# Kernel tuning notes

Hardware: AMD Instinct MI355X
Metric: run time of the kernel (lower is better)

The kernel has to match this reference:

```python
import jax, jax.numpy as jnp
import numpy as np

B, K, D = 32768, 64, 64
GAIN = 1.0
LOG_2PI = float(np.log(2.0 * np.pi))


def setup_inputs() -> dict:
    key = jax.random.key(0)
    k1, k2, k3, k4 = jax.random.split(key, 4)
    return {
        "x": jax.random.normal(k1, (B, D), jnp.float32),
        "means_raw": jax.random.normal(k2, (K, D), jnp.float32),
        "scale_raw": jax.random.normal(k3, (K, D, D), jnp.float32),
        "weights_raw": jax.random.normal(k4, (K,), jnp.float32),
    }


def reference(x, means_raw, scale_raw, weights_raw):
    # EqualizedLR reparametrization: w_eff = w * gain / sqrt(fan_in)
    means = means_raw * (GAIN / np.sqrt(K * D))              # [K, D]
    pre = scale_raw * (GAIN / np.sqrt(K * D * D))            # [K, D, D]
    # ExpScaleTril (diag=False): strict lower triangle + exp(diagonal)
    dvec = jnp.exp(jnp.diagonal(pre, axis1=-2, axis2=-1))    # [K, D]
    L = jnp.tril(pre, -1) + dvec[..., :, None] * jnp.eye(D, dtype=pre.dtype)  # [K, D, D]
    # mixture logits -> log weights (EqualizedLR then softmax parametrization)
    logw = jax.nn.log_softmax(weights_raw * (GAIN / np.sqrt(K)), axis=-1)    # [K]

    # Precompute L^{-1} per component (K,D small), then whiten via one big GEMM.
    eye = jnp.broadcast_to(jnp.eye(D, dtype=L.dtype), L.shape)
    Linv = jax.scipy.linalg.solve_triangular(L, eye, lower=True)             # [K, D, D]

    diff = x[:, None, :] - means[None, :, :]                 # [B, K, D]
    z = jnp.einsum('kij,bkj->bki', Linv, diff)               # whitened residuals [B, K, D]
    maha = jnp.sum(z * z, axis=-1)                           # [B, K]
    half_log_det = jnp.sum(jnp.log(dvec), axis=-1)           # [K]
    comp_lp = -0.5 * (maha + D * LOG_2PI) - half_log_det     # [B, K]

    lp = jax.scipy.special.logsumexp(comp_lp + logw, axis=-1)  # [B]
    return -jnp.mean(lp)
```

## Files before the change

kernel.cpp:

```cpp
#include <hip/hip_runtime.h>

#define LOG_2PI 1.8378770664093453f
#define LOG2E   1.4426950408889634f

typedef __attribute__((ext_vector_type(8))) short  short8;
typedef __attribute__((ext_vector_type(4))) float  float4_;
typedef __attribute__((ext_vector_type(4))) unsigned uint4_;

__device__ __forceinline__ unsigned short f2bf(float f) {
  unsigned u = __builtin_bit_cast(unsigned, f);
  u += 0x7fffu + ((u >> 16) & 1u);
  return (unsigned short)(u >> 16);
}
__device__ __forceinline__ float bf2f(unsigned short h) {
  return __builtin_bit_cast(float, ((unsigned)h) << 16);
}
__device__ __forceinline__ unsigned bits(float f) { return __builtin_bit_cast(unsigned, f); }
__device__ __forceinline__ float bitf(unsigned u) { return __builtin_bit_cast(float, u); }
__device__ __forceinline__ unsigned pk2(float lo, float hi) {
  return __builtin_amdgcn_perm(bits(hi), bits(lo), 0x07060302u);
}
__device__ __forceinline__ unsigned pk2r(float lo, float hi) {
  return __builtin_amdgcn_perm(bits(hi) + 0x8000u, bits(lo) + 0x8000u, 0x07060302u);
}
template <int CTRL>
__device__ __forceinline__ float dpp_add(float v) {
  int t = __builtin_amdgcn_mov_dpp(__builtin_bit_cast(int, v), CTRL, 0xf, 0xf, true);
  return v + __builtin_bit_cast(float, t);
}
__device__ __forceinline__ void async16(const void* g, void* l) {
  __builtin_amdgcn_global_load_lds((const __attribute__((address_space(1))) unsigned int*)g,
                                   (__attribute__((address_space(3))) unsigned int*)l, 16, 0, 0);
}


__global__ __launch_bounds__(256) void gmm_setup(
    const float* __restrict__ means_raw, const float* __restrict__ scale_raw,
    const float* __restrict__ weights_raw, unsigned short* __restrict__ Wv,
    float* __restrict__ out)
{
  const int k = blockIdx.x;
  const int t = threadIdx.x;
  const int lane = t & 63;
  const int wv = t >> 6;
  const int q = lane >> 4;
  const int jj = lane & 15;

  if (k == 0 && t == 0) out[0] = 0.0f;

  __shared__ float Plt[64][68];
  __shared__ float Vt[64][68];
  __shared__ __align__(16) unsigned short Vb[64][72];
  __shared__ float Msh[64][65];
  __shared__ float dg[64], rdg[64], mu_s[64], y_s[64], cs_[64];
  __shared__ float beta_s;

  {
    const int i = t >> 2;
    const int c0 = (t & 3) * 16;
    float4_ v4[4];
    const float4_* src = (const float4_*)(scale_raw + (size_t)k * 4096 + i * 64 + c0);
    v4[0] = src[0]; v4[1] = src[1]; v4[2] = src[2]; v4[3] = src[3];
#pragma unroll
    for (int e = 0; e < 16; ++e) {
      const int c = c0 + e;
      const float val = ((const float*)v4)[e] * (1.0f / 512.0f);
      Plt[c][i] = (c < i) ? val : 0.0f;
      if (c == i) { dg[i] = val; rdg[i] = __expf(-val); }
    }
  }
  if (t < 64) mu_s[t] = means_raw[k * 64 + t] * (1.0f / 64.0f);
  __syncthreads();

  {
    const int j = wv * 16 + jj;
    float s[16];
#pragma unroll
    for (int i = 0; i < 16; ++i) s[i] = 0.0f;
#pragma unroll
    for (int m = 0; m < 64; ++m) {
      const float rm = rdg[m];
      float vcand = (m == j) ? rm : -s[m & 15] * rm;
      const float v = __shfl(vcand, (m >> 4) * 16 + jj, 64);
      if (q == (m >> 4)) {
        Vt[j][m] = v;
        Vb[j][m] = f2bf(v);
      }
      const float4_* prow = (const float4_*)&Plt[m][16 * q];
      const float4_ p0 = prow[0], p1 = prow[1], p2 = prow[2], p3 = prow[3];
      s[0]  += p0[0] * v; s[1]  += p0[1] * v; s[2]  += p0[2] * v; s[3]  += p0[3] * v;
      s[4]  += p1[0] * v; s[5]  += p1[1] * v; s[6]  += p1[2] * v; s[7]  += p1[3] * v;
      s[8]  += p2[0] * v; s[9]  += p2[1] * v; s[10] += p2[2] * v; s[11] += p2[3] * v;
      s[12] += p3[0] * v; s[13] += p3[1] * v; s[14] += p3[2] * v; s[15] += p3[3] * v;
    }
  }
  __syncthreads();

  {
    const short8 a0 = *(const short8*)&Vb[16 * wv + jj][8 * q];
    const short8 a1 = *(const short8*)&Vb[16 * wv + jj][8 * q + 32];
#pragma unroll
    for (int t4 = 0; t4 < 4; ++t4) {
      const short8 b0 = *(const short8*)&Vb[jj + 16 * t4][8 * q];
      const short8 b1 = *(const short8*)&Vb[jj + 16 * t4][8 * q + 32];
      float4_ f = {0.f, 0.f, 0.f, 0.f};
      f = __builtin_amdgcn_mfma_f32_16x16x32_bf16(a0, b0, f, 0, 0, 0);
      f = __builtin_amdgcn_mfma_f32_16x16x32_bf16(a1, b1, f, 0, 0, 0);
#pragma unroll
      for (int r = 0; r < 4; ++r)
        Msh[16 * wv + 4 * q + r][jj + 16 * t4] = f[r];
    }
  }
  if (wv == 0) {
    float acc = 0.0f;
    for (int j2 = 0; j2 < 64; ++j2) acc += Vt[j2][lane] * mu_s[j2];
    y_s[lane] = acc;
  }
  __syncthreads();

  if (t < 64) {
    const int i = t;
    float ci = 0.0f;
#pragma unroll
    for (int m4 = 0; m4 < 16; ++m4) {
      const float4_ a4 = *(const float4_*)&Vt[i][4 * m4];
      const float4_ b4 = *(const float4_*)&y_s[4 * m4];
      ci += a4[0] * b4[0] + a4[1] * b4[1] + a4[2] * b4[2] + a4[3] * b4[3];
    }
    cs_[i] = LOG2E * ci;
    float rq  = ci * mu_s[i];
    float dgv = dg[i];
    const float wr = weights_raw[i] * 0.125f;
    float mx = wr;
#pragma unroll
    for (int d = 1; d < 64; d <<= 1) mx = fmaxf(mx, __shfl_xor(mx, d, 64));
    float se = __expf(wr - mx);
#pragma unroll
    for (int d = 1; d < 64; d <<= 1) {
      se  += __shfl_xor(se, d, 64);
      rq  += __shfl_xor(rq, d, 64);
      dgv += __shfl_xor(dgv, d, 64);
    }
    if (i == 0) {
      const float wrk  = weights_raw[k] * 0.125f;
      const float logw = wrk - mx - __logf(se);
      const float bval = -0.5f * rq - 32.0f * LOG_2PI - dgv + logw;
      beta_s = LOG2E * (bval + 90.0f);
    }
  }
  __syncthreads();

  {
    const int nt = k >> 4, lrk = k & 15;
    const int j = t & 7, qq = (t >> 3) & 3, cs = t >> 5;
    for (int it = 0; it < 10; ++it) {
      const int c = cs + 8 * it;
      if (c >= 76) break;
      float val = 0.0f;
      if (c < 72) {
        const int bp = c >> 1, ks = c & 1;
        int rb = bp, ib = 0;
        while (rb >= 8 - ib) { rb -= (8 - ib); ++ib; }
        const int jb = ib + rb;
        const int i = 8 * ib + 4 * ks + qq, j2 = 8 * jb + j;
        val = (ib == jb ? 1.0f : 2.0f) * (-0.5f * LOG2E) * Msh[i][j2];
      } else if (c == 72) {
        val = cs_[qq + 4 * j];
      } else if (c == 73) {
        val = cs_[qq + 32 + 4 * j];
      } else if (c == 74) {
        if (qq == 0 && j == 0) val = beta_s;
        else if (qq == 0 && j == 1) val = beta_s - bf2f(f2bf(beta_s));
      }
      Wv[(size_t)(c * 4 + nt) * 512 + (qq * 16 + lrk) * 8 + j] = f2bf(val);
    }
  }
}

__global__ __launch_bounds__(256) __attribute__((amdgpu_waves_per_eu(4, 4)))
void gmm_main(const float* __restrict__ x, const unsigned short* __restrict__ Wv,
              float* __restrict__ out)
{
  constexpr int IBt[36] = {0,0,0,0,0,0,0,0, 1,1,1,1,1,1,1, 2,2,2,2,2,2,
                           3,3,3,3,3, 4,4,4,4, 5,5,5, 6,6, 7};
  constexpr int JBt[36] = {0,1,2,3,4,5,6,7, 1,2,3,4,5,6,7, 2,3,4,5,6,7,
                           3,4,5,6,7, 4,5,6,7, 5,6,7, 6,7, 7};

  __shared__ __align__(16) unsigned short Wlds[2][8192];
  __shared__ float wsum[4];

  const int t = threadIdx.x;
  const int lane = t & 63;
  const int wv = t >> 6;
  const int q = lane >> 4;
  const int lr = lane & 15;
  const int row = blockIdx.x * 64 + wv * 16 + lr;

  unsigned xBp[32];
  {
    const float4_* xr4 = (const float4_*)(x + (size_t)row * 64);
#pragma unroll
    for (int m = 0; m < 16; ++m) {
      const float4_ v = xr4[m];
      xBp[2 * m]     = pk2r(v[0], v[1]);
      xBp[2 * m + 1] = pk2r(v[2], v[3]);
    }
  }
  unsigned xAp[8];
  {
    const float* xr = x + (size_t)row * 64 + q;
#pragma unroll
    for (int r = 0; r < 8; ++r)
      xAp[r] = pk2r(xr[8 * r], xr[8 * r + 4]);
  }

  float4_ f[4] = {{0,0,0,0},{0,0,0,0},{0,0,0,0},{0,0,0,0}};

#define STAGE(gg)                                                              \
  {                                                                            \
    const unsigned short* src = Wv + 8192 * (gg) + wv * 2048 + lane * 8;       \
    unsigned short* dst = &Wlds[(gg) & 1][0] + wv * 2048 + lane * 8;           \
    async16(src, dst);                 async16(src + 512, dst + 512);          \
    async16(src + 1024, dst + 1024);   async16(src + 1536, dst + 1536);        \
  }

  STAGE(0)
  __syncthreads();

#pragma unroll
  for (int g = 0; g < 19; ++g) {
    if (g < 18) STAGE(g + 1)
    const unsigned short* wb = &Wlds[g & 1][0];
#pragma unroll
    for (int cl = 0; cl < 4; ++cl) {
      const int c = 4 * g + cl;
      if (c >= 75) continue;
      short8 a;
      if (c < 72) {
        const int bp = c >> 1, ks = c & 1;
        const int ib = IBt[bp], jb = JBt[bp], tt = 2 * ib + ks;
        const unsigned ua = xAp[tt >> 1];
        const float xa = bitf((tt & 1) ? (ua & 0xffff0000u) : (ua << 16));
        uint4_ pk;
#pragma unroll
        for (int p = 0; p < 4; ++p) {
          const unsigned ub = xBp[4 * jb + p];
          const float b0 = bitf(ub << 16);
          const float b1 = bitf(ub & 0xffff0000u);
          pk[p] = pk2(xa * b0, xa * b1);
        }
        a = __builtin_bit_cast(short8, pk);
      } else if (c == 72) {
        uint4_ pk = {xAp[0], xAp[1], xAp[2], xAp[3]};
        a = __builtin_bit_cast(short8, pk);
      } else if (c == 73) {
        uint4_ pk = {xAp[4], xAp[5], xAp[6], xAp[7]};
        a = __builtin_bit_cast(short8, pk);
      } else {
        uint4_ pk = {0x3f803f80u, 0x3f803f80u, 0x3f803f80u, 0x3f803f80u};
        a = __builtin_bit_cast(short8, pk);
      }
#pragma unroll
      for (int nt = 0; nt < 4; ++nt) {
        const short8 b = *(const short8*)(wb + cl * 2048 + nt * 512 + lane * 8);
        f[nt] = __builtin_amdgcn_mfma_f32_16x16x32_bf16(a, b, f[nt], 0, 0, 0);
      }
    }
    __syncthreads();
  }
#undef STAGE

  float v = 0.0f;
  {
    float s[4];
#pragma unroll
    for (int r = 0; r < 4; ++r) {
      float e = exp2f(f[0][r]) + exp2f(f[1][r]) + exp2f(f[2][r]) + exp2f(f[3][r]);
      e = dpp_add<0x121>(e);
      e = dpp_add<0x122>(e);
      e = dpp_add<0x124>(e);
      e = dpp_add<0x128>(e);
      s[r] = e;
    }
    if (lr == 0)
      v = (__logf(s[0]) + __logf(s[1]) + __logf(s[2]) + __logf(s[3])) - 360.0f;
    v += __shfl_xor(v, 16, 64);
    v += __shfl_xor(v, 32, 64);
  }
  if (lane == 0) wsum[wv] = v;
  __syncthreads();
  if (t == 0)
    atomicAdd(out, -(wsum[0] + wsum[1] + wsum[2] + wsum[3]) * (1.0f / 32768.0f));
}

extern "C" void kernel_launch(void* const* d_in, const int* in_sizes, int n_in,
                              void* d_out, int out_size, void* d_ws, size_t ws_size,
                              hipStream_t stream)
{
  const float* x           = (const float*)d_in[0];
  const float* means_raw   = (const float*)d_in[1];
  const float* scale_raw   = (const float*)d_in[2];
  const float* weights_raw = (const float*)d_in[3];
  float* out = (float*)d_out;

  unsigned short* Wv = (unsigned short*)d_ws;

  gmm_setup<<<64, 256, 0, stream>>>(means_raw, scale_raw, weights_raw, Wv, out);
  gmm_main<<<512, 256, 0, stream>>>(x, Wv, out);
}
```

Baseline: 107.1 us.

## Stage six chunks per LDS buffer and vectorize setup weight writes

```diff
diff --git a/kernel.cpp b/kernel.cpp
--- a/kernel.cpp
+++ b/kernel.cpp
@@ -39,6 +39,11 @@
     const float* __restrict__ weights_raw, unsigned short* __restrict__ Wv,
     float* __restrict__ out)
 {
+  constexpr int IBt[36] = {0,0,0,0,0,0,0,0, 1,1,1,1,1,1,1, 2,2,2,2,2,2,
+                           3,3,3,3,3, 4,4,4,4, 5,5,5, 6,6, 7};
+  constexpr int JBt[36] = {0,1,2,3,4,5,6,7, 1,2,3,4,5,6,7, 2,3,4,5,6,7,
+                           3,4,5,6,7, 4,5,6,7, 5,6,7, 6,7, 7};
+
   const int k = blockIdx.x;
   const int t = threadIdx.x;
   const int lane = t & 63;
@@ -152,32 +157,44 @@
 
   {
     const int nt = k >> 4, lrk = k & 15;
-    const int j = t & 7, qq = (t >> 3) & 3, cs = t >> 5;
-    for (int it = 0; it < 10; ++it) {
-      const int c = cs + 8 * it;
-      if (c >= 76) break;
-      float val = 0.0f;
-      if (c < 72) {
-        const int bp = c >> 1, ks = c & 1;
-        int rb = bp, ib = 0;
-        while (rb >= 8 - ib) { rb -= (8 - ib); ++ib; }
-        const int jb = ib + rb;
-        const int i = 8 * ib + 4 * ks + qq, j2 = 8 * jb + j;
-        val = (ib == jb ? 1.0f : 2.0f) * (-0.5f * LOG2E) * Msh[i][j2];
-      } else if (c == 72) {
-        val = cs_[qq + 4 * j];
-      } else if (c == 73) {
-        val = cs_[qq + 32 + 4 * j];
-      } else if (c == 74) {
-        if (qq == 0 && j == 0) val = beta_s;
-        else if (qq == 0 && j == 1) val = beta_s - bf2f(f2bf(beta_s));
+#pragma unroll
+    for (int half = 0; half < 2; ++half) {
+      const int m = t + half * 256;
+      if (m < 312) {
+        const int c = m >> 2, qq = m & 3;
+        unsigned short h8[8];
+#pragma unroll
+        for (int e = 0; e < 8; ++e) h8[e] = 0;
+        if (c < 72) {
+          const int bp = c >> 1, ks = c & 1;
+          const int ib = IBt[bp], jb = JBt[bp];
+          const int i = 8 * ib + 4 * ks + qq;
+          const float sc = (ib == jb ? 1.0f : 2.0f) * (-0.5f * LOG2E);
+#pragma unroll
+          for (int e = 0; e < 8; ++e) h8[e] = f2bf(sc * Msh[i][8 * jb + e]);
+        } else if (c == 72) {
+#pragma unroll
+          for (int e = 0; e < 8; ++e) h8[e] = f2bf(cs_[qq + 4 * e]);
+        } else if (c == 73) {
+#pragma unroll
+          for (int e = 0; e < 8; ++e) h8[e] = f2bf(cs_[qq + 32 + 4 * e]);
+        } else if (c == 74) {
+          if (qq == 0) {
+            h8[0] = f2bf(beta_s);
+            h8[1] = f2bf(beta_s - bf2f(f2bf(beta_s)));
+          }
+        }
+        uint4_ pkd;
+#pragma unroll
+        for (int p = 0; p < 4; ++p)
+          pkd[p] = (unsigned)h8[2 * p] | ((unsigned)h8[2 * p + 1] << 16);
+        *(uint4_*)&Wv[(size_t)(c * 4 + nt) * 512 + (qq * 16 + lrk) * 8] = pkd;
       }
-      Wv[(size_t)(c * 4 + nt) * 512 + (qq * 16 + lrk) * 8 + j] = f2bf(val);
-    }
-  }
-}
-
-__global__ __launch_bounds__(256) __attribute__((amdgpu_waves_per_eu(4, 4)))
+    }
+  }
+}
+
+__global__ __launch_bounds__(256) __attribute__((amdgpu_waves_per_eu(2, 2)))
 void gmm_main(const float* __restrict__ x, const unsigned short* __restrict__ Wv,
               float* __restrict__ out)
 {
@@ -186,7 +203,7 @@
   constexpr int JBt[36] = {0,1,2,3,4,5,6,7, 1,2,3,4,5,6,7, 2,3,4,5,6,7,
                            3,4,5,6,7, 4,5,6,7, 5,6,7, 6,7, 7};
 
-  __shared__ __align__(16) unsigned short Wlds[2][8192];
+  __shared__ __align__(16) unsigned short Wlds[2][12288];
   __shared__ float wsum[4];
 
   const int t = threadIdx.x;
@@ -218,22 +235,23 @@
 
 #define STAGE(gg)                                                              \
   {                                                                            \
-    const unsigned short* src = Wv + 8192 * (gg) + wv * 2048 + lane * 8;       \
-    unsigned short* dst = &Wlds[(gg) & 1][0] + wv * 2048 + lane * 8;           \
-    async16(src, dst);                 async16(src + 512, dst + 512);          \
-    async16(src + 1024, dst + 1024);   async16(src + 1536, dst + 1536);        \
+    const unsigned short* src = Wv + 12288 * (gg) + t * 8;                     \
+    unsigned short* dst = &Wlds[(gg) & 1][0] + t * 8;                          \
+    async16(src, dst);                 async16(src + 2048,  dst + 2048);       \
+    async16(src + 4096,  dst + 4096);  async16(src + 6144,  dst + 6144);       \
+    async16(src + 8192,  dst + 8192);  async16(src + 10240, dst + 10240);      \
   }
 
   STAGE(0)
   __syncthreads();
 
 #pragma unroll
-  for (int g = 0; g < 19; ++g) {
-    if (g < 18) STAGE(g + 1)
+  for (int g = 0; g < 13; ++g) {
+    if (g < 12) STAGE(g + 1)
     const unsigned short* wb = &Wlds[g & 1][0];
 #pragma unroll
-    for (int cl = 0; cl < 4; ++cl) {
-      const int c = 4 * g + cl;
+    for (int cl = 0; cl < 6; ++cl) {
+      const int c = 6 * g + cl;
       if (c >= 75) continue;
       short8 a;
       if (c < 72) {
```

New measurement: 97.97 us. 8.5% less time.
